# Kernel optimization log

Hardware: AMD Instinct MI355X
Metric: run time of the kernel (lower is better)

Reference implementation:

```python
import jax, jax.numpy as jnp
import numpy as np

NUM_HEADS = 4
CHUNK = 64
GATE_NORM = 16.0
EPS = 1e-5


def _xavier(key, fan_in, fan_out):
    gain = 2.0 ** (-2.5)
    limit = gain * np.sqrt(6.0 / (fan_in + fan_out))
    return jax.random.uniform(key, (fan_in, fan_out), jnp.float32, -limit, limit)


def setup_inputs() -> dict:
    key = jax.random.key(0)
    ks = jax.random.split(key, 8)
    B, L, D = 4, 2048, 1024
    Dk, Dv, R = 1024, 2048, 16
    x = jax.random.normal(ks[0], (B, L, D), jnp.float32)
    return {
        "x": x,
        "Wq": _xavier(ks[1], D, Dk),
        "Wk": _xavier(ks[2], D, Dk),
        "Wv": _xavier(ks[3], D, Dv),
        "Wg": _xavier(ks[4], D, Dv),
        "gk_w1": _xavier(ks[5], D, R),
        "gk_w2": _xavier(ks[6], R, Dk),
        "gk_b2": jnp.zeros((Dk,), jnp.float32),
        "g_norm_w": jnp.ones((Dv // NUM_HEADS,), jnp.float32),
        "Wo": _xavier(ks[7], Dv, D),
    }


def _to_chunks(t, B, H, NC, C):
    # [B,H,L,d] -> [NC,B,H,C,d]
    d = t.shape[-1]
    return t.reshape(B, H, NC, C, d).transpose(2, 0, 1, 3, 4)


def _gla_forward(x, Wq, Wk, Wv, Wg, gk_w1, gk_w2, gk_b2, g_norm_w, Wo):
    B, L, D = x.shape
    H = NUM_HEADS
    C = CHUNK
    NC = L // C

    q = x @ Wq  # [B,L,Dk]
    k = x @ Wk
    v = x @ Wv  # [B,L,Dv]
    gk = jax.nn.log_sigmoid((x @ gk_w1) @ gk_w2 + gk_b2) / GATE_NORM  # [B,L,Dk]

    def split_heads(t):
        return t.reshape(B, L, H, -1).transpose(0, 2, 1, 3)  # [B,H,L,d]

    q, k, v, gk = map(split_heads, (q, k, v, gk))
    dk = q.shape[-1]
    scale = dk ** -0.5

    qc = _to_chunks(q, B, H, NC, C)
    kc = _to_chunks(k, B, H, NC, C)
    vc = _to_chunks(v, B, H, NC, C)
    gc = _to_chunks(gk, B, H, NC, C)
    Bcum = jnp.cumsum(gc, axis=3)  # inclusive log-decay within chunk

    causal = jnp.tril(jnp.ones((C, C), jnp.float32))  # s <= t

    def step(Hst, inp):
        qi, ki, vi, bi = inp  # [B,H,C,dk/dv]
        qg = qi * jnp.exp(bi) * scale           # q_t * exp(B_t)
        kg = ki * jnp.exp(-bi)                  # k_s * exp(-B_s)
        o_inter = jnp.einsum('bhcd,bhde->bhce', qg, Hst)
        A = jnp.einsum('bhtd,bhsd->bhts', qg, kg) * causal
        o_intra = jnp.einsum('bhts,bhse->bhte', A, vi)
        b_last = bi[:, :, -1:, :]               # total chunk decay [B,H,1,dk]
        kH = ki * jnp.exp(b_last - bi)          # decay remaining after s
        H_new = jnp.exp(b_last).transpose(0, 1, 3, 2) * Hst + \
            jnp.einsum('bhcd,bhce->bhde', kH, vi)
        return H_new, o_inter + o_intra

    dv = v.shape[-1]
    H0 = jnp.zeros((B, H, dk, dv), jnp.float32)
    _, oc = jax.lax.scan(step, H0, (qc, kc, vc, Bcum))  # [NC,B,H,C,dv]
    o = oc.transpose(1, 2, 0, 3, 4).reshape(B, H, L, dv)
    o = o.transpose(0, 2, 1, 3)  # [B,L,H,dv]

    # FusedRMSNormSwishGate: RMSNorm(o) * w * swish(g)
    rms = jnp.sqrt(jnp.mean(o * o, axis=-1, keepdims=True) + EPS)
    o_n = (o / rms) * g_norm_w
    g = (x @ Wg).reshape(B, L, H, dv)
    o = o_n * g * jax.nn.sigmoid(g)
    return o.reshape(B, L, H * dv) @ Wo


def reference(x, Wq, Wk, Wv, Wg, gk_w1, gk_w2, gk_b2, g_norm_w, Wo):
    return _gla_forward(x, Wq, Wk, Wv, Wg, gk_w1, gk_w2, gk_b2, g_norm_w, Wo)
```

## Files before the change

### kernel.cpp

```cpp
#include <hip/hip_runtime.h>
#include <hip/hip_bf16.h>

typedef __attribute__((ext_vector_type(8))) __bf16 bf16x8;
typedef __attribute__((ext_vector_type(4))) __bf16 bf16x4;
typedef __attribute__((ext_vector_type(4))) float f32x4;

#define MFMA16(a, b, c) __builtin_amdgcn_mfma_f32_16x16x32_bf16((a), (b), (c), 0, 0, 0)

__device__ __forceinline__ void gload_lds16(const void* g, void* l) {
    __builtin_amdgcn_global_load_lds((const __attribute__((address_space(1))) void*)g,
                                     (__attribute__((address_space(3))) void*)l, 16, 0, 0);
}

__global__ __launch_bounds__(256) void cvt_bf16(const float* __restrict__ in,
                                                __bf16* __restrict__ out, int n4) {
    int i = blockIdx.x * 256 + threadIdx.x;
    if (i >= n4) return;
    f32x4 v = *(const f32x4*)(in + (size_t)i * 4);
    bf16x4 o;
#pragma unroll
    for (int j = 0; j < 4; j++) o[j] = (__bf16)v[j];
    *(bf16x4*)(out + (size_t)i * 4) = o;
}

__global__ __launch_bounds__(256) void transpose_w(const float* __restrict__ in,
                                                   __bf16* __restrict__ out, int R, int C) {
    __shared__ float tile[32][33];
    const int c0 = blockIdx.x * 32, r0 = blockIdx.y * 32;
    const int tx = threadIdx.x, ty = threadIdx.y;
#pragma unroll
    for (int k = 0; k < 32; k += 8)
        tile[ty + k][tx] = in[(size_t)(r0 + ty + k) * C + c0 + tx];
    __syncthreads();
#pragma unroll
    for (int k = 0; k < 32; k += 8)
        out[(size_t)(c0 + ty + k) * R + r0 + tx] = (__bf16)tile[tx][ty + k];
}

template <typename OUT_T>
__global__ __launch_bounds__(256) void gemm_bt(const __bf16* __restrict__ A,
                                               const __bf16* __restrict__ Bt,
                                               OUT_T* __restrict__ C, int M, int N, int K) {
    __shared__ alignas(16) __bf16 As[4096];
    __shared__ alignas(16) __bf16 Bs[4096];
    const int tid = threadIdx.x;
    const int wv = tid >> 6;
    const int nwg = gridDim.x;
    const int cpx = nwg >> 3;
    const int bid = blockIdx.x;
    const int wg = (bid & 7) * cpx + (bid >> 3);
    const int nbn = N >> 7;
    const int bm = wg / nbn, bn = wg - bm * nbn;

    const __bf16* Ab = A + (size_t)bm * 128 * K;
    const __bf16* Bb = Bt + (size_t)bn * 128 * K;
    const int srow = tid >> 2;
    const int skc = (tid & 3) * 8;
    const int lr = tid & 15;
    const int lk = ((tid >> 4) & 3) * 8;
    const int wm = (wv >> 1) * 64, wn = (wv & 1) * 64;

    f32x4 acc[4][4] = {};
    for (int kt = 0; kt < K; kt += 32) {
        gload_lds16(Ab + (size_t)srow * K + kt + skc, As + wv * 512);
        gload_lds16(Ab + (size_t)(srow + 64) * K + kt + skc, As + 2048 + wv * 512);
        gload_lds16(Bb + (size_t)srow * K + kt + skc, Bs + wv * 512);
        gload_lds16(Bb + (size_t)(srow + 64) * K + kt + skc, Bs + 2048 + wv * 512);
        asm volatile("s_waitcnt vmcnt(0)" ::: "memory");
        __syncthreads();
        bf16x8 af[4], bfr[4];
#pragma unroll
        for (int i = 0; i < 4; i++) af[i] = *(const bf16x8*)(As + (wm + i * 16 + lr) * 32 + lk);
#pragma unroll
        for (int j = 0; j < 4; j++) bfr[j] = *(const bf16x8*)(Bs + (wn + j * 16 + lr) * 32 + lk);
#pragma unroll
        for (int i = 0; i < 4; i++)
#pragma unroll
            for (int j = 0; j < 4; j++) acc[i][j] = MFMA16(af[i], bfr[j], acc[i][j]);
        __syncthreads();
    }
    const int lro = ((tid >> 4) & 3) * 4;
#pragma unroll
    for (int i = 0; i < 4; i++)
#pragma unroll
        for (int j = 0; j < 4; j++) {
            size_t base = (size_t)(bm * 128 + wm + i * 16 + lro) * N + bn * 128 + wn + j * 16 + lr;
#pragma unroll
            for (int r = 0; r < 4; r++) C[base + (size_t)r * N] = (OUT_T)acc[i][j][r];
        }
}

__global__ __launch_bounds__(256) void gk1_proj(const float* __restrict__ x,
                                                const float* __restrict__ w1,
                                                float* __restrict__ t) {
    const int row = blockIdx.x * 4 + (threadIdx.x >> 6);
    const int l = threadIdx.x & 63;
    const int r = l & 15, kg = l >> 4;
    const float* xr = x + (size_t)row * 1024;
    const float* w1p = w1 + r;
    float acc = 0.f;
    for (int k = kg * 256; k < (kg + 1) * 256; ++k) acc = fmaf(xr[k], w1p[k * 16], acc);
    acc += __shfl_xor(acc, 16);
    acc += __shfl_xor(acc, 32);
    if (kg == 0) t[(size_t)row * 16 + r] = acc;
}

__global__ __launch_bounds__(1024, 4) void gate_qkg(
    const float* __restrict__ tbuf,
    const float* __restrict__ w2,
    const float* __restrict__ b2,
    const __bf16* __restrict__ qkbuf,
    __bf16* __restrict__ qg,
    __bf16* __restrict__ kg,
    __bf16* __restrict__ kgT,
    float* __restrict__ ebl)
{
    __shared__ alignas(16) float t_l[128 * 16];
    __shared__ float qs[4 * 256];
    __shared__ __bf16 kg_l[128 * 260];
    const int bid = blockIdx.x;
    const int bh = bid & 15, nc = bid >> 4;
    const int b = bh >> 2, h = bh & 3;
    const int tid = threadIdx.x;
    const int d = tid & 255, cq = tid >> 8;
    const int seq0 = b * 2048 + nc * 128;
    const int hd = h * 256 + d;

    for (int i = tid; i < 128 * 16; i += 1024) t_l[i] = tbuf[(size_t)seq0 * 16 + i];
    float w2c[16];
#pragma unroll
    for (int r = 0; r < 16; r++) w2c[r] = w2[r * 1024 + hd];
    const float b2v = b2[hd];
    __syncthreads();

    float bs[32];
    float run = 0.f;
#pragma unroll
    for (int j = 0; j < 32; j++) {
        const int c = cq * 32 + j;
        f32x4 t0 = *(const f32x4*)(t_l + c * 16);
        f32x4 t1 = *(const f32x4*)(t_l + c * 16 + 4);
        f32x4 t2 = *(const f32x4*)(t_l + c * 16 + 8);
        f32x4 t3 = *(const f32x4*)(t_l + c * 16 + 12);
        float u = b2v;
#pragma unroll
        for (int r = 0; r < 4; r++) {
            u = fmaf(t0[r], w2c[r], u);
            u = fmaf(t1[r], w2c[4 + r], u);
            u = fmaf(t2[r], w2c[8 + r], u);
            u = fmaf(t3[r], w2c[12 + r], u);
        }
        const float ls = fminf(u, 0.f) - __logf(1.f + __expf(-fabsf(u)));
        run += ls * 0.0625f;
        bs[j] = run;
    }
    qs[cq * 256 + d] = run;
    __syncthreads();

    float prefix = 0.f;
#pragma unroll
    for (int q = 0; q < 3; q++)
        if (q < cq) prefix += qs[q * 256 + d];

#pragma unroll
    for (int j = 0; j < 32; j++) {
        const int c = cq * 32 + j;
        const float bsum = prefix + bs[j];
        const float eb = __expf(bsum);
        const float en = __expf(-bsum);
        const float qv = (float)qkbuf[(size_t)(seq0 + c) * 2048 + hd];
        const float kv = (float)qkbuf[(size_t)(seq0 + c) * 2048 + 1024 + hd];
        qg[(size_t)(seq0 + c) * 1024 + hd] = (__bf16)(qv * eb * 0.0625f);
        const __bf16 kgv = (__bf16)(kv * en);
        kg[(size_t)(seq0 + c) * 1024 + hd] = kgv;
        kg_l[c * 260 + d] = kgv;
    }
    if (cq == 3) ebl[(size_t)(nc * 16 + bh) * 256 + d] = __expf(prefix + bs[31]);
    __syncthreads();

    {
        const int cc = tid & 127, dgroup = tid >> 7;
        for (int i = 0; i < 32; i++) {
            const int dd = dgroup * 32 + i;
            kgT[(size_t)(bh * 256 + dd) * 2048 + nc * 128 + cc] = kg_l[cc * 260 + dd];
        }
    }
}

__global__ __launch_bounds__(512) void a_mat(
    const __bf16* __restrict__ qg, const __bf16* __restrict__ kg,
    __bf16* __restrict__ Abuf) {
    const int pair = blockIdx.x;
    const int bh = pair & 15, nc = pair >> 4;
    const int b = bh >> 2, h = bh & 3;
    const int tid = threadIdx.x, wv = tid >> 6, l = tid & 63;
    const int lr = l & 15, lk = (l >> 4) * 8, lro = (l >> 4) * 4;
    const int seq0 = b * 2048 + nc * 128;
    __bf16* Ab = Abuf + (size_t)pair * 16384;

    {
        bf16x8 z = {};
        for (int i = tid; i < 2048; i += 512) *(bf16x8*)(Ab + (size_t)i * 8) = z;
    }
    __syncthreads();

    static const int TJ[36] = {0,1,1,2,2,2,3,3,3,3,4,4,4,4,4,5,5,5,5,5,5,
                               6,6,6,6,6,6,6,7,7,7,7,7,7,7,7};
    static const int TS[36] = {0,0,1,0,1,2,0,1,2,3,0,1,2,3,4,0,1,2,3,4,5,
                               0,1,2,3,4,5,6,0,1,2,3,4,5,6,7};
    for (int m = wv; m < 36; m += 8) {
        const int j = TJ[m], s = TS[m];
        f32x4 acc = {};
        const __bf16* qrow = qg + (size_t)(seq0 + j * 16 + lr) * 1024 + h * 256;
        const __bf16* krow = kg + (size_t)(seq0 + s * 16 + lr) * 1024 + h * 256;
#pragma unroll
        for (int ks = 0; ks < 8; ks++) {
            bf16x8 a = *(const bf16x8*)(qrow + ks * 32 + lk);
            bf16x8 bb = *(const bf16x8*)(krow + ks * 32 + lk);
            acc = MFMA16(a, bb, acc);
        }
#pragma unroll
        for (int r = 0; r < 4; r++) {
            const int t = j * 16 + lro + r;
            const int ss = s * 16 + lr;
            if (ss <= t) Ab[t * 128 + ss] = (__bf16)acc[r];
        }
    }
}

__global__ __launch_bounds__(256) void ointer(
    const __bf16* __restrict__ Abuf, const __bf16* __restrict__ qg,
    const __bf16* __restrict__ vt, const __bf16* __restrict__ UH,
    __bf16* __restrict__ ob) {
    __shared__ alignas(16) __bf16 As[4096];
    __shared__ alignas(16) __bf16 Bs[4096];
    const int tid = threadIdx.x;
    const int wv = tid >> 6;
    const int bid = blockIdx.x;
    const int wg = (bid & 7) * 128 + (bid >> 3);
    const int bn = wg & 3, pair = wg >> 2;
    const int bh = pair & 15, nc = pair >> 4;
    const int b = bh >> 2, h = bh & 3;
    const int seq0 = b * 2048 + nc * 128;
    const int srow = tid >> 2;
    const int skc = (tid & 3) * 8;
    const int lr = tid & 15;
    const int lk = ((tid >> 4) & 3) * 8;
    const int wm = (wv >> 1) * 64, wn = (wv & 1) * 64;
    const int KE = (nc == 0) ? 128 : 384;

    const __bf16* Ap = Abuf + (size_t)pair * 16384;
    const __bf16* Hb = UH + ((size_t)((nc - 1) * 16 + bh) * 512 + bn * 128) * 256;

    f32x4 acc[4][4] = {};
    for (int kt = 0; kt < KE; kt += 32) {
        const __bf16 *a0, *a1, *b0, *b1;
        if (kt < 128) {
            a0 = Ap + srow * 128 + kt + skc;
            a1 = Ap + (srow + 64) * 128 + kt + skc;
            b0 = vt + (size_t)(h * 512 + bn * 128 + srow) * 8192 + seq0 + kt + skc;
            b1 = vt + (size_t)(h * 512 + bn * 128 + srow + 64) * 8192 + seq0 + kt + skc;
        } else {
            const int kd = kt - 128;
            a0 = qg + (size_t)(seq0 + srow) * 1024 + h * 256 + kd + skc;
            a1 = qg + (size_t)(seq0 + srow + 64) * 1024 + h * 256 + kd + skc;
            b0 = Hb + (size_t)srow * 256 + kd + skc;
            b1 = Hb + (size_t)(srow + 64) * 256 + kd + skc;
        }
        gload_lds16(a0, As + wv * 512);
        gload_lds16(a1, As + 2048 + wv * 512);
        gload_lds16(b0, Bs + wv * 512);
        gload_lds16(b1, Bs + 2048 + wv * 512);
        asm volatile("s_waitcnt vmcnt(0)" ::: "memory");
        __syncthreads();
        bf16x8 af[4], bfr[4];
#pragma unroll
        for (int i = 0; i < 4; i++) af[i] = *(const bf16x8*)(As + (wm + i * 16 + lr) * 32 + lk);
#pragma unroll
        for (int j = 0; j < 4; j++) bfr[j] = *(const bf16x8*)(Bs + (wn + j * 16 + lr) * 32 + lk);
#pragma unroll
        for (int i = 0; i < 4; i++)
#pragma unroll
            for (int j = 0; j < 4; j++) acc[i][j] = MFMA16(af[i], bfr[j], acc[i][j]);
        __syncthreads();
    }
    const int lro = ((tid >> 4) & 3) * 4;
#pragma unroll
    for (int i = 0; i < 4; i++)
#pragma unroll
        for (int j = 0; j < 4; j++) {
            size_t base = (size_t)(seq0 + wm + i * 16 + lro) * 2048 + h * 512 + bn * 128 + wn + j * 16 + lr;
#pragma unroll
            for (int r = 0; r < 4; r++) ob[base + (size_t)r * 2048] = (__bf16)acc[i][j][r];
        }
}

__global__ __launch_bounds__(512) void chunk_u(
    const __bf16* __restrict__ vt, const __bf16* __restrict__ kgT,
    __bf16* __restrict__ UH) {
    const int bid = blockIdx.x;
    const int bh = bid & 15, nc = (bid >> 4) & 15, q = bid >> 8;
    const int eh = q >> 1, dh = q & 1;
    const int b = bh >> 2, h = bh & 3;
    const int tid = threadIdx.x, wv = tid >> 6, l = tid & 63;
    const int lr = l & 15, lk = (l >> 4) * 8, lro = (l >> 4) * 4;
    const int seq0 = b * 2048 + nc * 128;
    const int e0 = eh * 256 + (wv >> 1) * 64;
    const int d0 = dh * 128 + (wv & 1) * 64;
    const __bf16* va = vt + (size_t)(h * 512 + e0) * 8192 + seq0;
    const __bf16* kb = kgT + (size_t)(bh * 256 + d0) * 2048 + nc * 128;

    f32x4 acc[4][4] = {};
#pragma unroll
    for (int ks = 0; ks < 4; ks++) {
        bf16x8 af[4], bf_[4];
#pragma unroll
        for (int i = 0; i < 4; i++)
            af[i] = *(const bf16x8*)(va + (size_t)(i * 16 + lr) * 8192 + ks * 32 + lk);
#pragma unroll
        for (int j = 0; j < 4; j++)
            bf_[j] = *(const bf16x8*)(kb + (size_t)(j * 16 + lr) * 2048 + ks * 32 + lk);
#pragma unroll
        for (int i = 0; i < 4; i++)
#pragma unroll
            for (int j = 0; j < 4; j++) acc[i][j] = MFMA16(af[i], bf_[j], acc[i][j]);
    }
    __bf16* ub = UH + ((size_t)(nc * 16 + bh) * 512 + e0) * 256 + d0;
#pragma unroll
    for (int i = 0; i < 4; i++)
#pragma unroll
        for (int j = 0; j < 4; j++)
#pragma unroll
            for (int r = 0; r < 4; r++)
                ub[(size_t)(i * 16 + lro + r) * 256 + j * 16 + lr] = (__bf16)acc[i][j][r];
}

__global__ __launch_bounds__(256) void hscan(__bf16* __restrict__ UH,
                                             const float* __restrict__ ebl) {
    const int t = blockIdx.x * 256 + threadIdx.x;
    const int bh = t >> 14;
    const int rem = t & 16383;
    const int e = rem >> 5, d0 = (rem & 31) * 8;
    float H[8];
#pragma unroll
    for (int j = 0; j < 8; j++) H[j] = 0.f;
    for (int i = 0; i < 16; i++) {
        size_t idx = ((size_t)(i * 16 + bh) * 512 + e) * 256 + d0;
        bf16x8 u = *(const bf16x8*)(UH + idx);
        const float* ep = ebl + (size_t)(i * 16 + bh) * 256 + d0;
        f32x4 e0v = *(const f32x4*)ep;
        f32x4 e1v = *(const f32x4*)(ep + 4);
        bf16x8 hw;
#pragma unroll
        for (int j = 0; j < 4; j++) {
            H[j] = e0v[j] * (H[j] + (float)u[j]);
            hw[j] = (__bf16)H[j];
        }
#pragma unroll
        for (int j = 4; j < 8; j++) {
            H[j] = e1v[j - 4] * (H[j] + (float)u[j]);
            hw[j] = (__bf16)H[j];
        }
        *(bf16x8*)(UH + idx) = hw;
    }
}

__global__ __launch_bounds__(256) void rms_gate(const __bf16* __restrict__ ob,
                                                const __bf16* __restrict__ gbuf,
                                                const float* __restrict__ gnw,
                                                __bf16* __restrict__ gated) {
    const int idx = blockIdx.x * 4 + (threadIdx.x >> 6);
    const int seq = idx >> 2, h = idx & 3;
    const int l = threadIdx.x & 63;
    bf16x8 o1 = *(const bf16x8*)(ob + (size_t)seq * 2048 + h * 512 + l * 8);
    float v[8];
    float ms = 0.f;
#pragma unroll
    for (int j = 0; j < 8; j++) {
        v[j] = (float)o1[j];
        ms += v[j] * v[j];
    }
#pragma unroll
    for (int off = 1; off < 64; off <<= 1) ms += __shfl_xor(ms, off);
    const float rinv = rsqrtf(ms * (1.f / 512.f) + 1e-5f);
    bf16x8 gv = *(const bf16x8*)(gbuf + (size_t)seq * 2048 + h * 512 + l * 8);
    const float* gw = gnw + l * 8;
    bf16x8 outv;
#pragma unroll
    for (int j = 0; j < 8; j++) {
        float g = (float)gv[j];
        float sig = 1.f / (1.f + expf(-g));
        outv[j] = (__bf16)(v[j] * rinv * gw[j] * g * sig);
    }
    *(bf16x8*)(gated + (size_t)seq * 2048 + h * 512 + l * 8) = outv;
}

extern "C" void kernel_launch(void* const* d_in, const int* in_sizes, int n_in,
                              void* d_out, int out_size, void* d_ws, size_t ws_size,
                              hipStream_t stream) {
    const float* x = (const float*)d_in[0];
    const float* Wq = (const float*)d_in[1];
    const float* Wk = (const float*)d_in[2];
    const float* Wv = (const float*)d_in[3];
    const float* Wg = (const float*)d_in[4];
    const float* w1 = (const float*)d_in[5];
    const float* w2 = (const float*)d_in[6];
    const float* b2 = (const float*)d_in[7];
    const float* gnw = (const float*)d_in[8];
    const float* Wo = (const float*)d_in[9];
    float* out = (float*)d_out;

    char* p = (char*)d_ws;
    auto nxt = [&](size_t bytes) {
        char* r = p;
        p += (bytes + 255) & ~(size_t)255;
        return r;
    };
    __bf16* xb = (__bf16*)nxt(8192ull * 1024 * 2);
    __bf16* WTqk = (__bf16*)nxt(2048ull * 1024 * 2);
    __bf16* WTg = (__bf16*)nxt(2048ull * 1024 * 2);
    __bf16* WvT = (__bf16*)nxt(2048ull * 1024 * 2);
    __bf16* WoT = (__bf16*)nxt(1024ull * 2048 * 2);
    __bf16* gbuf = (__bf16*)nxt(8192ull * 2048 * 2);
    __bf16* vt = (__bf16*)nxt(2048ull * 8192 * 2);
    float* tbuf = (float*)nxt(8192ull * 16 * 4);
    __bf16* qg = (__bf16*)nxt(8192ull * 1024 * 2);
    __bf16* kgT = (__bf16*)nxt(16ull * 256 * 2048 * 2);
    float* ebl = (float*)nxt(16ull * 16 * 256 * 4);
    __bf16* ob = (__bf16*)nxt(8192ull * 2048 * 2);
    __bf16* UH = (__bf16*)nxt(16ull * 16 * 512 * 256 * 2);
    __bf16* kg = xb;
    __bf16* qkbuf = UH;
    __bf16* gated = UH;
    __bf16* Abuf = WTqk;

    dim3 tb(32, 8);
    cvt_bf16<<<8192, 256, 0, stream>>>(x, xb, 2097152);
    transpose_w<<<dim3(32, 32), tb, 0, stream>>>(Wq, WTqk, 1024, 1024);
    transpose_w<<<dim3(32, 32), tb, 0, stream>>>(Wk, WTqk + 1024 * 1024, 1024, 1024);
    transpose_w<<<dim3(64, 32), tb, 0, stream>>>(Wg, WTg, 1024, 2048);
    transpose_w<<<dim3(64, 32), tb, 0, stream>>>(Wv, WvT, 1024, 2048);
    transpose_w<<<dim3(32, 64), tb, 0, stream>>>(Wo, WoT, 2048, 1024);
    gk1_proj<<<2048, 256, 0, stream>>>(x, w1, tbuf);
    gemm_bt<__bf16><<<1024, 256, 0, stream>>>(xb, WTqk, qkbuf, 8192, 2048, 1024);
    gemm_bt<__bf16><<<1024, 256, 0, stream>>>(xb, WTg, gbuf, 8192, 2048, 1024);
    gemm_bt<__bf16><<<1024, 256, 0, stream>>>(WvT, xb, vt, 2048, 8192, 1024);
    gate_qkg<<<256, 1024, 0, stream>>>(tbuf, w2, b2, qkbuf, qg, kg, kgT, ebl);
    a_mat<<<256, 512, 0, stream>>>(qg, kg, Abuf);
    chunk_u<<<1024, 512, 0, stream>>>(vt, kgT, UH);
    hscan<<<1024, 256, 0, stream>>>(UH, ebl);
    ointer<<<1024, 256, 0, stream>>>(Abuf, qg, vt, UH, ob);
    rms_gate<<<8192, 256, 0, stream>>>(ob, gbuf, gnw, gated);
    gemm_bt<float><<<512, 256, 0, stream>>>(gated, WoT, out, 8192, 1024, 2048);
}
```

Measured before the change: 432.1 us.

## Triple-buffer LDS in bf16 GEMM to overlap global loads with MFMA

The GEMM main loop now uses three LDS buffers with two stages prefetched ahead through direct global-to-LDS loads. It waits with partial vmcnt so the tile for step t can be consumed while the loads for steps t+1 and t+2 are still in flight. This drops one of the two barriers per iteration and is meant to hide global memory latency behind the MFMA work. LDS use triples to 48KB per block, which may lower occupancy, and the correctness of buffer reuse depends on the single barrier's placement.

After: 420.2 us. 2.7% less time.

```diff
diff --git a/kernel.cpp b/kernel.cpp
--- a/kernel.cpp
+++ b/kernel.cpp
@@ -41,8 +41,8 @@
 __global__ __launch_bounds__(256) void gemm_bt(const __bf16* __restrict__ A,
                                                const __bf16* __restrict__ Bt,
                                                OUT_T* __restrict__ C, int M, int N, int K) {
-    __shared__ alignas(16) __bf16 As[4096];
-    __shared__ alignas(16) __bf16 Bs[4096];
+    __shared__ alignas(16) __bf16 As[3][4096];
+    __shared__ alignas(16) __bf16 Bs[3][4096];
     const int tid = threadIdx.x;
     const int wv = tid >> 6;
     const int nwg = gridDim.x;
@@ -60,24 +60,45 @@
     const int lk = ((tid >> 4) & 3) * 8;
     const int wm = (wv >> 1) * 64, wn = (wv & 1) * 64;
 
+    auto STAGE = [&](int buf, int kt) {
+        gload_lds16(Ab + (size_t)srow * K + kt + skc, &As[buf][0] + wv * 512);
+        gload_lds16(Ab + (size_t)(srow + 64) * K + kt + skc, &As[buf][0] + 2048 + wv * 512);
+        gload_lds16(Bb + (size_t)srow * K + kt + skc, &Bs[buf][0] + wv * 512);
+        gload_lds16(Bb + (size_t)(srow + 64) * K + kt + skc, &Bs[buf][0] + 2048 + wv * 512);
+    };
+
+    const int nt = K >> 5;
+    STAGE(0, 0);
+    STAGE(1, 32);
+
     f32x4 acc[4][4] = {};
-    for (int kt = 0; kt < K; kt += 32) {
-        gload_lds16(Ab + (size_t)srow * K + kt + skc, As + wv * 512);
-        gload_lds16(Ab + (size_t)(srow + 64) * K + kt + skc, As + 2048 + wv * 512);
-        gload_lds16(Bb + (size_t)srow * K + kt + skc, Bs + wv * 512);
-        gload_lds16(Bb + (size_t)(srow + 64) * K + kt + skc, Bs + 2048 + wv * 512);
-        asm volatile("s_waitcnt vmcnt(0)" ::: "memory");
-        __syncthreads();
+    int buf = 0;
+    for (int t = 0; t < nt; ++t) {
+        asm volatile("s_waitcnt lgkmcnt(0)" ::: "memory");
+        if (t + 1 < nt)
+            asm volatile("s_waitcnt vmcnt(4)" ::: "memory");
+        else
+            asm volatile("s_waitcnt vmcnt(0)" ::: "memory");
+        __builtin_amdgcn_s_barrier();
+        __builtin_amdgcn_sched_barrier(0);
+        if (t + 2 < nt) {
+            int nb = buf + 2;
+            if (nb >= 3) nb -= 3;
+            STAGE(nb, (t + 2) * 32);
+        }
+        const __bf16* as = &As[buf][0];
+        const __bf16* bs = &Bs[buf][0];
         bf16x8 af[4], bfr[4];
 #pragma unroll
-        for (int i = 0; i < 4; i++) af[i] = *(const bf16x8*)(As + (wm + i * 16 + lr) * 32 + lk);
-#pragma unroll
-        for (int j = 0; j < 4; j++) bfr[j] = *(const bf16x8*)(Bs + (wn + j * 16 + lr) * 32 + lk);
+        for (int i = 0; i < 4; i++) af[i] = *(const bf16x8*)(as + (wm + i * 16 + lr) * 32 + lk);
+#pragma unroll
+        for (int j = 0; j < 4; j++) bfr[j] = *(const bf16x8*)(bs + (wn + j * 16 + lr) * 32 + lk);
 #pragma unroll
         for (int i = 0; i < 4; i++)
 #pragma unroll
             for (int j = 0; j < 4; j++) acc[i][j] = MFMA16(af[i], bfr[j], acc[i][j]);
-        __syncthreads();
+        buf += 1;
+        if (buf >= 3) buf -= 3;
     }
     const int lro = ((tid >> 4) & 3) * 4;
 #pragma unroll
```
